# Performance work log

Hardware: AMD Instinct MI355X
Metric: run time of the kernel (lower is better)

Reference implementation:

```python
import jax, jax.numpy as jnp
import numpy as np
from jax import lax

H, W, C = 24, 8, 128
HW = H * W
PART = 4
SA_K = 49  # CBAM spatial-attention kernel size (default of CBAMBlock)
EPS = 1e-5


def conv2d(x, w, b, pad_h, pad_w):
    y = lax.conv_general_dilated(x, w, (1, 1), [(pad_h, pad_h), (pad_w, pad_w)],
                                 dimension_numbers=('NCHW', 'OIHW', 'NCHW'))
    return y + b[None, :, None, None]


def cbam(x, se_w1, se_w2, sa_w, sa_b):
    # Channel attention: shared MLP on global max- and avg-pooled descriptors.
    mx = x.max(axis=(2, 3))          # [n, c]
    av = x.mean(axis=(2, 3))         # [n, c]
    def se(v):
        return jax.nn.relu(v @ se_w1.T) @ se_w2.T
    ca = jax.nn.sigmoid(se(mx) + se(av))[:, :, None, None]
    out = x * ca
    # Spatial attention: 49x49 conv on [max, mean] over channels.
    smx = out.max(axis=1, keepdims=True)
    sav = out.mean(axis=1, keepdims=True)
    s = jnp.concatenate([smx, sav], axis=1)      # [n, 2, H, W]
    sa = jax.nn.sigmoid(conv2d(s, sa_w, sa_b, SA_K // 2, SA_K // 2))
    return out * sa + x


def position_aware_max(score6, dim):
    # score6: [p, g, hr, wr, hs, ws]; fixed-length (part_rows) row window,
    # start clamped to [0, h - part_rows] -> vectorized sliding-window max.
    part_rows = H // PART
    half = part_rows // 2
    starts = jnp.clip(jnp.arange(H) - half, 0, H - part_rows)
    if dim == 0:
        m = score6.max(axis=3)            # max over wr -> [p, g, hr, hs, ws]
        mi = jnp.moveaxis(m, 3, 0)        # [hs, p, g, hr, ws]
        def f(m_i, st):
            return lax.dynamic_slice_in_dim(m_i, st, part_rows, axis=2).max(axis=2)
        out = jax.vmap(f)(mi, starts)     # [h, p, g, ws]
    else:
        m = score6.max(axis=5)            # max over ws -> [p, g, hr, wr, hs]
        mi = jnp.moveaxis(m, 2, 0)        # [hr, p, g, wr, hs]
        def f(m_i, st):
            return lax.dynamic_slice_in_dim(m_i, st, part_rows, axis=3).max(axis=3)
        out = jax.vmap(f)(mi, starts)     # [h, p, g, wr]
    p, g = score6.shape[0], score6.shape[1]
    return jnp.moveaxis(out, 0, 2).reshape(p, g, HW)


def bn_eval(x, gamma, beta, mean, var):
    return (x - mean) * (gamma / jnp.sqrt(var + EPS)) + beta


def setup_inputs() -> dict:
    key = jax.random.key(0)
    ks = jax.random.split(key, 8)
    red = 16
    return {
        'prob_fea': jax.random.normal(ks[0], (32, C, H, W), jnp.float32),
        'gal_fea': jax.random.normal(ks[1], (32, C, H, W), jnp.float32),
        'se_w1': jax.random.normal(ks[2], (C // red, C), jnp.float32) * 0.05,
        'se_w2': jax.random.normal(ks[3], (C, C // red), jnp.float32) * 0.05,
        'sa_w': jax.random.normal(ks[4], (1, 2, SA_K, SA_K), jnp.float32) * 0.02,
        'sa_b': jnp.zeros((1,), jnp.float32),
        'bn_g': jnp.ones((1,), jnp.float32),
        'bn_b': jnp.zeros((1,), jnp.float32),
        'bn_m': jnp.zeros((1,), jnp.float32),
        'bn_v': jnp.ones((1,), jnp.float32),
        'fc_w': jnp.full((1, HW), 1.0 / HW, jnp.float32),
        'fc_b': jax.random.normal(ks[5], (1,), jnp.float32) * 0.01,
        'lbn_g': jnp.ones((1,), jnp.float32),
        'lbn_b': jnp.zeros((1,), jnp.float32),
        'lbn_m': jnp.zeros((1,), jnp.float32),
        'lbn_v': jnp.ones((1,), jnp.float32),
    }


def reference(prob_fea, gal_fea, se_w1, se_w2, sa_w, sa_b,
              bn_g, bn_b, bn_m, bn_v, fc_w, fc_b,
              lbn_g, lbn_b, lbn_m, lbn_v):
    pf = cbam(prob_fea, se_w1, se_w2, sa_w, sa_b)
    gf = cbam(gal_fea, se_w1, se_w2, sa_w, sa_b)
    p, g = pf.shape[0], gf.shape[0]
    pf = pf.reshape(p, C, HW)
    gf = gf.reshape(g, C, HW)
    # pairwise feature matching: [p, g, r(gal spatial), s(prob spatial)]
    score = jnp.einsum('pcs,gcr->pgrs', pf, gf)
    score6 = score.reshape(p, g, H, W, H, W)
    s1 = position_aware_max(score6, 0)  # [p, g, HW]
    s2 = position_aware_max(score6, 1)  # [p, g, HW]
    sc = jnp.concatenate([s1, s2], axis=-1).reshape(-1, HW)  # [p*g*2, HW]
    sc = bn_eval(sc, bn_g, bn_b, bn_m, bn_v)
    y = sc @ fc_w.T + fc_b                  # [p*g*2, 1]
    y = y.reshape(-1, 2).sum(axis=1, keepdims=True)
    y = bn_eval(y, lbn_g, lbn_b, lbn_m, lbn_v)
    return jax.nn.sigmoid(y).reshape(p, g)
```

## Files before the change

### kernel.cpp

```cpp
#include <hip/hip_runtime.h>
#include <hip/hip_bf16.h>

#define HH 24
#define WW 8
#define HWSZ 192
#define CC 128
#define EPSV 1e-5f

#define M1LD 200
#define M2LD 28

typedef __attribute__((ext_vector_type(8))) short bf16x8;
typedef __attribute__((ext_vector_type(4))) float f32x4;

__device__ __forceinline__ float sigmoidf_(float x) { return 1.0f / (1.0f + expf(-x)); }

__device__ __forceinline__ unsigned short f2bf(float f) {
    unsigned int u = __float_as_uint(f);
    unsigned int r = (u + 0x7fffu + ((u >> 16) & 1u)) >> 16;
    return (unsigned short)r;
}
__device__ __forceinline__ float bf2f(unsigned short s) {
    return __uint_as_float((unsigned int)s << 16);
}

__global__ __launch_bounds__(512) void cbam_stats(
    const float* __restrict__ prob, const float* __restrict__ gal,
    const float* __restrict__ se_w1, const float* __restrict__ se_w2,
    const float* __restrict__ sa_w, const float* __restrict__ sa_b,
    float* __restrict__ ca_out, float* __restrict__ sa_out)
{
    __shared__ float mxs[CC], avs[CC], hid[16], cas[CC];
    __shared__ float smx2[2 * HWSZ], sav2[2 * HWSZ];
    __shared__ float wbuf[2 * 49 * 49];

    int n = blockIdx.x;
    const float* x = (n < 32) ? prob + (size_t)n * CC * HWSZ : gal + (size_t)(n - 32) * CC * HWSZ;

    int tid = threadIdx.x, l = tid & 63, w = tid >> 6;

    for (int i = tid; i < 2 * 49 * 49; i += 512) wbuf[i] = sa_w[i];

    for (int i = 0; i < 16; ++i) {
        int c = w * 16 + i;
        const float* row = x + c * HWSZ;
        float a = row[l], b = row[l + 64], d = row[l + 128];
        float mv = fmaxf(a, fmaxf(b, d));
        float sv = a + b + d;
        #pragma unroll
        for (int m = 1; m < 64; m <<= 1) {
            mv = fmaxf(mv, __shfl_xor(mv, m));
            sv += __shfl_xor(sv, m);
        }
        if (l == 0) { mxs[c] = mv; avs[c] = sv * (1.0f / HWSZ); }
    }
    __syncthreads();

    if (tid < 256) {
        int j = tid >> 4, chunk = tid & 15;
        const float* v = (j < 8) ? mxs : avs;
        const float* wrow = se_w1 + (j & 7) * CC + chunk * 8;
        const float* vv = v + chunk * 8;
        float acc = 0.f;
        #pragma unroll
        for (int k = 0; k < 8; ++k) acc += vv[k] * wrow[k];
        #pragma unroll
        for (int m = 1; m < 16; m <<= 1) acc += __shfl_xor(acc, m);
        if (chunk == 0) hid[j] = fmaxf(acc, 0.f);
    }
    __syncthreads();

    if (tid < CC) {
        float acc = 0.f;
        #pragma unroll
        for (int j = 0; j < 8; ++j) acc += (hid[j] + hid[8 + j]) * se_w2[tid * 8 + j];
        cas[tid] = sigmoidf_(acc);
        ca_out[n * CC + tid] = cas[tid];
    }
    __syncthreads();

    if (tid < 2 * HWSZ) {
        int s = tid >> 1, half = tid & 1;
        int c0 = half * 64;
        float mv = -INFINITY, sv = 0.f;
        #pragma unroll 4
        for (int k = 0; k < 64; ++k) {
            float v = x[(c0 + k) * HWSZ + s] * cas[c0 + k];
            mv = fmaxf(mv, v); sv += v;
        }
        smx2[half * HWSZ + s] = mv; sav2[half * HWSZ + s] = sv;
    }
    __syncthreads();

    if (tid < HWSZ) {
        int y = tid >> 3, xx = tid & 7;
        float acc = sa_b[0];
        for (int iy = 0; iy < HH; ++iy) {
            int wy = iy - y + 24;
            const float* w0 = wbuf + wy * 49;
            const float* w1 = wbuf + 2401 + wy * 49;
            #pragma unroll
            for (int ix = 0; ix < WW; ++ix) {
                int wx = ix - xx + 24;
                int sp = iy * 8 + ix;
                float s0 = fmaxf(smx2[sp], smx2[HWSZ + sp]);
                float s1 = (sav2[sp] + sav2[HWSZ + sp]) * (1.0f / CC);
                acc += s0 * w0[wx] + s1 * w1[wx];
            }
        }
        sa_out[n * HWSZ + tid] = sigmoidf_(acc);
    }
}

__global__ __launch_bounds__(256) void cbam_apply(
    const float* __restrict__ prob, const float* __restrict__ gal,
    const float* __restrict__ ca_buf, const float* __restrict__ sa_buf,
    __hip_bfloat16* __restrict__ pf_t, __hip_bfloat16* __restrict__ gf_t)
{
    __shared__ unsigned short T[16][136];
    __shared__ float sash[16];

    int n = blockIdx.x / 12;
    int s0 = (blockIdx.x % 12) * 16;
    const float* x = (n < 32) ? prob + (size_t)n * CC * HWSZ : gal + (size_t)(n - 32) * CC * HWSZ;
    __hip_bfloat16* dst = (n < 32) ? pf_t + (size_t)n * HWSZ * CC : gf_t + (size_t)(n - 32) * HWSZ * CC;

    int tid = threadIdx.x;
    if (tid < 16) sash[tid] = sa_buf[n * HWSZ + s0 + tid];
    __syncthreads();

    int c = tid >> 1, half = tid & 1;
    float ca = ca_buf[n * CC + c];
    const float* xp = x + c * HWSZ + s0 + half * 8;
    float4 va = *(const float4*)xp;
    float4 vb = *(const float4*)(xp + 4);
    int r0 = half * 8;
    T[r0 + 0][c] = f2bf(va.x * (1.f + ca * sash[r0 + 0]));
    T[r0 + 1][c] = f2bf(va.y * (1.f + ca * sash[r0 + 1]));
    T[r0 + 2][c] = f2bf(va.z * (1.f + ca * sash[r0 + 2]));
    T[r0 + 3][c] = f2bf(va.w * (1.f + ca * sash[r0 + 3]));
    T[r0 + 4][c] = f2bf(vb.x * (1.f + ca * sash[r0 + 4]));
    T[r0 + 5][c] = f2bf(vb.y * (1.f + ca * sash[r0 + 5]));
    T[r0 + 6][c] = f2bf(vb.z * (1.f + ca * sash[r0 + 6]));
    T[r0 + 7][c] = f2bf(vb.w * (1.f + ca * sash[r0 + 7]));
    __syncthreads();

    int s_l = tid >> 4, c8 = (tid & 15) * 8;
    const unsigned int* src = (const unsigned int*)&T[s_l][c8];
    unsigned int* d32 = (unsigned int*)(dst + (s0 + s_l) * CC + c8);
    d32[0] = src[0]; d32[1] = src[1]; d32[2] = src[2]; d32[3] = src[3];
}

__global__ __launch_bounds__(384) void score_kernel(
    const __hip_bfloat16* __restrict__ pf_t, const __hip_bfloat16* __restrict__ gf_t,
    const float* __restrict__ bn_g, const float* __restrict__ bn_b,
    const float* __restrict__ bn_m, const float* __restrict__ bn_v,
    const float* __restrict__ fc_w, const float* __restrict__ fc_b,
    const float* __restrict__ lbn_g, const float* __restrict__ lbn_b,
    const float* __restrict__ lbn_m, const float* __restrict__ lbn_v,
    float* __restrict__ out)
{
    __shared__ __align__(16) char Bs[12 * 4096];
    __shared__ unsigned short M1b[24 * M1LD];
    __shared__ unsigned short M2b[HWSZ * M2LD];
    __shared__ float red[6], wred[6];

    int bi = blockIdx.x;
    int p = bi >> 5, g = bi & 31;
    int tid = threadIdx.x, l = tid & 63, w = tid >> 6;

    const __hip_bfloat16* A = gf_t + (size_t)g * HWSZ * CC;
    const __hip_bfloat16* B = pf_t + (size_t)p * HWSZ * CC;

    #pragma unroll
    for (int i = 0; i < 8; ++i) {
        int idx = w * 8 + i;
        const __hip_bfloat16* src = B + ((idx >> 2) * 16 + (l & 15)) * CC
                                      + ((idx & 3) * 4 + (l >> 4)) * 8;
        __builtin_amdgcn_global_load_lds(
            (const __attribute__((address_space(1))) void*)src,
            (__attribute__((address_space(3))) void*)(&Bs[idx * 1024]),
            16, 0, 0);
    }

    int row_a = l & 15;
    int koff = (l >> 4) * 8;
    bf16x8 afr[2][4];
    #pragma unroll
    for (int rt = 0; rt < 2; ++rt) {
        const __hip_bfloat16* ap = A + (w * 32 + rt * 16 + row_a) * CC + koff;
        #pragma unroll
        for (int ks = 0; ks < 4; ++ks)
            afr[rt][ks] = *(const bf16x8*)(ap + ks * 32);
    }
    __syncthreads();

    for (int st = 0; st < 12; ++st) {
        const char* bb = Bs + st * 4096;
        bf16x8 b0 = *(const bf16x8*)(bb + 0 * 1024 + l * 16);
        bf16x8 b1 = *(const bf16x8*)(bb + 1 * 1024 + l * 16);
        bf16x8 b2 = *(const bf16x8*)(bb + 2 * 1024 + l * 16);
        bf16x8 b3 = *(const bf16x8*)(bb + 3 * 1024 + l * 16);

        #pragma unroll
        for (int rt = 0; rt < 2; ++rt) {
            f32x4 acc1 = {0.f, 0.f, 0.f, 0.f};
            f32x4 acc2 = {0.f, 0.f, 0.f, 0.f};
            acc1 = __builtin_amdgcn_mfma_f32_16x16x32_bf16(afr[rt][0], b0, acc1, 0, 0, 0);
            acc2 = __builtin_amdgcn_mfma_f32_16x16x32_bf16(b0, afr[rt][0], acc2, 0, 0, 0);
            acc1 = __builtin_amdgcn_mfma_f32_16x16x32_bf16(afr[rt][1], b1, acc1, 0, 0, 0);
            acc2 = __builtin_amdgcn_mfma_f32_16x16x32_bf16(b1, afr[rt][1], acc2, 0, 0, 0);
            acc1 = __builtin_amdgcn_mfma_f32_16x16x32_bf16(afr[rt][2], b2, acc1, 0, 0, 0);
            acc2 = __builtin_amdgcn_mfma_f32_16x16x32_bf16(b2, afr[rt][2], acc2, 0, 0, 0);
            acc1 = __builtin_amdgcn_mfma_f32_16x16x32_bf16(afr[rt][3], b3, acc1, 0, 0, 0);
            acc2 = __builtin_amdgcn_mfma_f32_16x16x32_bf16(b3, afr[rt][3], acc2, 0, 0, 0);

            int RT = w * 2 + rt;

            float mrow = fmaxf(fmaxf(acc1[0], acc1[1]), fmaxf(acc1[2], acc1[3]));
            mrow = fmaxf(mrow, __shfl_xor(mrow, 16));
            if (((l >> 4) & 1) == 0)
                M1b[(2 * RT + (l >> 5)) * M1LD + st * 16 + (l & 15)] = f2bf(mrow);

            float mcol = fmaxf(fmaxf(acc2[0], acc2[1]), fmaxf(acc2[2], acc2[3]));
            mcol = fmaxf(mcol, __shfl_xor(mcol, 16));
            if (((l >> 4) & 1) == 0)
                M2b[(RT * 16 + (l & 15)) * M2LD + st * 2 + (l >> 5)] = f2bf(mcol);
        }
    }
    __syncthreads();

    float part = 0.f, wpart = 0.f;
    if (tid < HWSZ) {
        int h = tid >> 3;
        int st0 = h - 3; if (st0 < 0) st0 = 0; if (st0 > 18) st0 = 18;
        float v1 = -INFINITY, v2 = -INFINITY;
        #pragma unroll
        for (int i = 0; i < 6; ++i) {
            v1 = fmaxf(v1, bf2f(M1b[(st0 + i) * M1LD + tid]));
            v2 = fmaxf(v2, bf2f(M2b[tid * M2LD + st0 + i]));
        }
        float fw = fc_w[tid];
        part = fw * (v1 + v2);
        wpart = fw;
    }
    #pragma unroll
    for (int m = 1; m < 64; m <<= 1) {
        part  += __shfl_xor(part, m);
        wpart += __shfl_xor(wpart, m);
    }
    if (l == 0) { red[w] = part; wred[w] = wpart; }
    __syncthreads();

    if (tid == 0) {
        float total = red[0] + red[1] + red[2] + red[3] + red[4] + red[5];
        float Wsum  = wred[0] + wred[1] + wred[2] + wred[3] + wred[4] + wred[5];
        float k1 = bn_g[0] * rsqrtf(bn_v[0] + EPSV);
        float Y = k1 * total + 2.f * ((bn_b[0] - k1 * bn_m[0]) * Wsum + fc_b[0]);
        float kl = lbn_g[0] * rsqrtf(lbn_v[0] + EPSV);
        float Z = (Y - lbn_m[0]) * kl + lbn_b[0];
        out[bi] = 1.f / (1.f + expf(-Z));
    }
}

extern "C" void kernel_launch(void* const* d_in, const int* in_sizes, int n_in,
                              void* d_out, int out_size, void* d_ws, size_t ws_size,
                              hipStream_t stream)
{
    const float* prob  = (const float*)d_in[0];
    const float* gal   = (const float*)d_in[1];
    const float* se_w1 = (const float*)d_in[2];
    const float* se_w2 = (const float*)d_in[3];
    const float* sa_w  = (const float*)d_in[4];
    const float* sa_b  = (const float*)d_in[5];
    const float* bn_g  = (const float*)d_in[6];
    const float* bn_b  = (const float*)d_in[7];
    const float* bn_m  = (const float*)d_in[8];
    const float* bn_v  = (const float*)d_in[9];
    const float* fc_w  = (const float*)d_in[10];
    const float* fc_b  = (const float*)d_in[11];
    const float* lbn_g = (const float*)d_in[12];
    const float* lbn_b = (const float*)d_in[13];
    const float* lbn_m = (const float*)d_in[14];
    const float* lbn_v = (const float*)d_in[15];

    __hip_bfloat16* pf_t = (__hip_bfloat16*)d_ws;
    __hip_bfloat16* gf_t = pf_t + (size_t)32 * HWSZ * CC;
    float* ca_buf = (float*)(gf_t + (size_t)32 * HWSZ * CC);
    float* sa_buf = ca_buf + 64 * CC;
    float* out = (float*)d_out;

    cbam_stats<<<64, 512, 0, stream>>>(prob, gal, se_w1, se_w2, sa_w, sa_b, ca_buf, sa_buf);
    cbam_apply<<<768, 256, 0, stream>>>(prob, gal, ca_buf, sa_buf, pf_t, gf_t);
    score_kernel<<<1024, 384, 0, stream>>>(pf_t, gf_t, bn_g, bn_b, bn_m, bn_v,
                                           fc_w, fc_b, lbn_g, lbn_b, lbn_m, lbn_v, out);
}
```

Before: 151.8 us.

## Switch score GEMM to 32x32x16 MFMA with direct global B loads

The score kernel now uses 32x32x16 bf16 MFMA tiles instead of 16x16x32. Each wave covers 32 gallery rows against 32-position prob tiles over 6 steps. The LDS staging buffer for the prob features is removed, so B fragments are read straight from global memory (likely L2-resident) and the leading barrier goes away. It also adds an occupancy hint to launch_bounds. The intent is fewer MFMA issues, less LDS use and higher occupancy, at the cost of more global-load latency inside the inner loop and a larger accumulator register footprint.

```diff
diff --git a/kernel.cpp b/kernel.cpp
--- a/kernel.cpp
+++ b/kernel.cpp
@@ -11,7 +11,7 @@
 #define M2LD 28
 
 typedef __attribute__((ext_vector_type(8))) short bf16x8;
-typedef __attribute__((ext_vector_type(4))) float f32x4;
+typedef __attribute__((ext_vector_type(16))) float f32x16;
 
 __device__ __forceinline__ float sigmoidf_(float x) { return 1.0f / (1.0f + expf(-x)); }
 
@@ -151,7 +151,7 @@
     d32[0] = src[0]; d32[1] = src[1]; d32[2] = src[2]; d32[3] = src[3];
 }
 
-__global__ __launch_bounds__(384) void score_kernel(
+__global__ __launch_bounds__(384, 4) void score_kernel(
     const __hip_bfloat16* __restrict__ pf_t, const __hip_bfloat16* __restrict__ gf_t,
     const float* __restrict__ bn_g, const float* __restrict__ bn_b,
     const float* __restrict__ bn_m, const float* __restrict__ bn_v,
@@ -160,7 +160,6 @@
     const float* __restrict__ lbn_m, const float* __restrict__ lbn_v,
     float* __restrict__ out)
 {
-    __shared__ __align__(16) char Bs[12 * 4096];
     __shared__ unsigned short M1b[24 * M1LD];
     __shared__ unsigned short M2b[HWSZ * M2LD];
     __shared__ float red[6], wred[6];
@@ -172,60 +171,53 @@
     const __hip_bfloat16* A = gf_t + (size_t)g * HWSZ * CC;
     const __hip_bfloat16* B = pf_t + (size_t)p * HWSZ * CC;
 
-    #pragma unroll
-    for (int i = 0; i < 8; ++i) {
-        int idx = w * 8 + i;
-        const __hip_bfloat16* src = B + ((idx >> 2) * 16 + (l & 15)) * CC
-                                      + ((idx & 3) * 4 + (l >> 4)) * 8;
-        __builtin_amdgcn_global_load_lds(
-            (const __attribute__((address_space(1))) void*)src,
-            (__attribute__((address_space(3))) void*)(&Bs[idx * 1024]),
-            16, 0, 0);
-    }
-
-    int row_a = l & 15;
-    int koff = (l >> 4) * 8;
-    bf16x8 afr[2][4];
-    #pragma unroll
-    for (int rt = 0; rt < 2; ++rt) {
-        const __hip_bfloat16* ap = A + (w * 32 + rt * 16 + row_a) * CC + koff;
-        #pragma unroll
-        for (int ks = 0; ks < 4; ++ks)
-            afr[rt][ks] = *(const bf16x8*)(ap + ks * 32);
-    }
-    __syncthreads();
-
-    for (int st = 0; st < 12; ++st) {
-        const char* bb = Bs + st * 4096;
-        bf16x8 b0 = *(const bf16x8*)(bb + 0 * 1024 + l * 16);
-        bf16x8 b1 = *(const bf16x8*)(bb + 1 * 1024 + l * 16);
-        bf16x8 b2 = *(const bf16x8*)(bb + 2 * 1024 + l * 16);
-        bf16x8 b3 = *(const bf16x8*)(bb + 3 * 1024 + l * 16);
-
-        #pragma unroll
-        for (int rt = 0; rt < 2; ++rt) {
-            f32x4 acc1 = {0.f, 0.f, 0.f, 0.f};
-            f32x4 acc2 = {0.f, 0.f, 0.f, 0.f};
-            acc1 = __builtin_amdgcn_mfma_f32_16x16x32_bf16(afr[rt][0], b0, acc1, 0, 0, 0);
-            acc2 = __builtin_amdgcn_mfma_f32_16x16x32_bf16(b0, afr[rt][0], acc2, 0, 0, 0);
-            acc1 = __builtin_amdgcn_mfma_f32_16x16x32_bf16(afr[rt][1], b1, acc1, 0, 0, 0);
-            acc2 = __builtin_amdgcn_mfma_f32_16x16x32_bf16(b1, afr[rt][1], acc2, 0, 0, 0);
-            acc1 = __builtin_amdgcn_mfma_f32_16x16x32_bf16(afr[rt][2], b2, acc1, 0, 0, 0);
-            acc2 = __builtin_amdgcn_mfma_f32_16x16x32_bf16(b2, afr[rt][2], acc2, 0, 0, 0);
-            acc1 = __builtin_amdgcn_mfma_f32_16x16x32_bf16(afr[rt][3], b3, acc1, 0, 0, 0);
-            acc2 = __builtin_amdgcn_mfma_f32_16x16x32_bf16(b3, afr[rt][3], acc2, 0, 0, 0);
-
-            int RT = w * 2 + rt;
-
-            float mrow = fmaxf(fmaxf(acc1[0], acc1[1]), fmaxf(acc1[2], acc1[3]));
-            mrow = fmaxf(mrow, __shfl_xor(mrow, 16));
-            if (((l >> 4) & 1) == 0)
-                M1b[(2 * RT + (l >> 5)) * M1LD + st * 16 + (l & 15)] = f2bf(mrow);
-
-            float mcol = fmaxf(fmaxf(acc2[0], acc2[1]), fmaxf(acc2[2], acc2[3]));
-            mcol = fmaxf(mcol, __shfl_xor(mcol, 16));
-            if (((l >> 4) & 1) == 0)
-                M2b[(RT * 16 + (l & 15)) * M2LD + st * 2 + (l >> 5)] = f2bf(mcol);
+    int r32 = l & 31;
+    int koff = (l >> 5) * 8;
+
+    bf16x8 afr[8];
+    {
+        const __hip_bfloat16* ap = A + (w * 32 + r32) * CC + koff;
+        #pragma unroll
+        for (int ks = 0; ks < 8; ++ks) afr[ks] = *(const bf16x8*)(ap + ks * 16);
+    }
+
+    const __hip_bfloat16* bp0 = B + r32 * CC + koff;
+
+    for (int st = 0; st < 6; ++st) {
+        const __hip_bfloat16* bp = bp0 + st * 32 * CC;
+        f32x16 acc1 = {};
+        f32x16 acc2 = {};
+        #pragma unroll
+        for (int ks = 0; ks < 8; ++ks) {
+            bf16x8 bfr = *(const bf16x8*)(bp + ks * 16);
+            acc1 = __builtin_amdgcn_mfma_f32_32x32x16_bf16(afr[ks], bfr, acc1, 0, 0, 0);
+            acc2 = __builtin_amdgcn_mfma_f32_32x32x16_bf16(bfr, afr[ks], acc2, 0, 0, 0);
+        }
+
+        #pragma unroll
+        for (int q = 0; q < 4; ++q) {
+            float m = fmaxf(fmaxf(acc1[4 * q + 0], acc1[4 * q + 1]),
+                            fmaxf(acc1[4 * q + 2], acc1[4 * q + 3]));
+            m = fmaxf(m, __shfl_xor(m, 32));
+            if (l < 32)
+                M1b[(w * 4 + q) * M1LD + st * 32 + l] = f2bf(m);
+        }
+
+        unsigned short pk0, pk1, pk2, pk3;
+        {
+            float m0 = fmaxf(fmaxf(acc2[0], acc2[1]), fmaxf(acc2[2], acc2[3]));
+            float m1 = fmaxf(fmaxf(acc2[4], acc2[5]), fmaxf(acc2[6], acc2[7]));
+            float m2 = fmaxf(fmaxf(acc2[8], acc2[9]), fmaxf(acc2[10], acc2[11]));
+            float m3 = fmaxf(fmaxf(acc2[12], acc2[13]), fmaxf(acc2[14], acc2[15]));
+            m0 = fmaxf(m0, __shfl_xor(m0, 32));
+            m1 = fmaxf(m1, __shfl_xor(m1, 32));
+            m2 = fmaxf(m2, __shfl_xor(m2, 32));
+            m3 = fmaxf(m3, __shfl_xor(m3, 32));
+            pk0 = f2bf(m0); pk1 = f2bf(m1); pk2 = f2bf(m2); pk3 = f2bf(m3);
+        }
+        if (l < 32) {
+            ushort4 v; v.x = pk0; v.y = pk1; v.z = pk2; v.w = pk3;
+            *(ushort4*)(&M2b[(w * 32 + l) * M2LD + st * 4]) = v;
         }
     }
     __syncthreads();
```

Measured after the change: 155.3 us. 2.3% more time.

## Double-buffer probe feature staging in LDS and raise occupancy hint

Applied to the files above, without the earlier changes.

Replaces the single 48KB LDS load of the whole probe feature tile with a two-buffer ring of 12KB groups. The next group is prefetched while MFMAs run on the current one. This shrinks LDS per block so more blocks fit per CU, and the launch bound now requests 4 waves-per-EU occupancy. The cost is a barrier per group and possible register pressure from the occupancy hint.

```diff
diff --git a/kernel.cpp b/kernel.cpp
--- a/kernel.cpp
+++ b/kernel.cpp
@@ -151,7 +151,7 @@
     d32[0] = src[0]; d32[1] = src[1]; d32[2] = src[2]; d32[3] = src[3];
 }
 
-__global__ __launch_bounds__(384) void score_kernel(
+__global__ __launch_bounds__(384, 4) void score_kernel(
     const __hip_bfloat16* __restrict__ pf_t, const __hip_bfloat16* __restrict__ gf_t,
     const float* __restrict__ bn_g, const float* __restrict__ bn_b,
     const float* __restrict__ bn_m, const float* __restrict__ bn_v,
@@ -160,7 +160,7 @@
     const float* __restrict__ lbn_m, const float* __restrict__ lbn_v,
     float* __restrict__ out)
 {
-    __shared__ __align__(16) char Bs[12 * 4096];
+    __shared__ __align__(16) char bstage[2][3 * 4096];
     __shared__ unsigned short M1b[24 * M1LD];
     __shared__ unsigned short M2b[HWSZ * M2LD];
     __shared__ float red[6], wred[6];
@@ -172,16 +172,22 @@
     const __hip_bfloat16* A = gf_t + (size_t)g * HWSZ * CC;
     const __hip_bfloat16* B = pf_t + (size_t)p * HWSZ * CC;
 
-    #pragma unroll
-    for (int i = 0; i < 8; ++i) {
-        int idx = w * 8 + i;
-        const __hip_bfloat16* src = B + ((idx >> 2) * 16 + (l & 15)) * CC
-                                      + ((idx & 3) * 4 + (l >> 4)) * 8;
-        __builtin_amdgcn_global_load_lds(
-            (const __attribute__((address_space(1))) void*)src,
-            (__attribute__((address_space(3))) void*)(&Bs[idx * 1024]),
-            16, 0, 0);
-    }
+    #define STAGE_G(buf_, grp_)                                                          \
+        {                                                                                \
+            _Pragma("unroll")                                                            \
+            for (int i_ = 0; i_ < 2; ++i_) {                                             \
+                int idx_ = w * 2 + i_;                 \
+                const __hip_bfloat16* src_ = B + (((grp_) * 3 + (idx_ >> 2)) * 16        \
+                                                  + (l & 15)) * CC                       \
+                                               + ((idx_ & 3) * 4 + (l >> 4)) * 8;        \
+                __builtin_amdgcn_global_load_lds(                                        \
+                    (const __attribute__((address_space(1))) void*)src_,                 \
+                    (__attribute__((address_space(3))) void*)(&bstage[buf_][idx_ * 1024]),\
+                    16, 0, 0);                                                           \
+            }                                                                            \
+        }
+
+    STAGE_G(0, 0)
 
     int row_a = l & 15;
     int koff = (l >> 4) * 8;
@@ -195,40 +201,47 @@
     }
     __syncthreads();
 
-    for (int st = 0; st < 12; ++st) {
-        const char* bb = Bs + st * 4096;
-        bf16x8 b0 = *(const bf16x8*)(bb + 0 * 1024 + l * 16);
-        bf16x8 b1 = *(const bf16x8*)(bb + 1 * 1024 + l * 16);
-        bf16x8 b2 = *(const bf16x8*)(bb + 2 * 1024 + l * 16);
-        bf16x8 b3 = *(const bf16x8*)(bb + 3 * 1024 + l * 16);
-
-        #pragma unroll
-        for (int rt = 0; rt < 2; ++rt) {
-            f32x4 acc1 = {0.f, 0.f, 0.f, 0.f};
-            f32x4 acc2 = {0.f, 0.f, 0.f, 0.f};
-            acc1 = __builtin_amdgcn_mfma_f32_16x16x32_bf16(afr[rt][0], b0, acc1, 0, 0, 0);
-            acc2 = __builtin_amdgcn_mfma_f32_16x16x32_bf16(b0, afr[rt][0], acc2, 0, 0, 0);
-            acc1 = __builtin_amdgcn_mfma_f32_16x16x32_bf16(afr[rt][1], b1, acc1, 0, 0, 0);
-            acc2 = __builtin_amdgcn_mfma_f32_16x16x32_bf16(b1, afr[rt][1], acc2, 0, 0, 0);
-            acc1 = __builtin_amdgcn_mfma_f32_16x16x32_bf16(afr[rt][2], b2, acc1, 0, 0, 0);
-            acc2 = __builtin_amdgcn_mfma_f32_16x16x32_bf16(b2, afr[rt][2], acc2, 0, 0, 0);
-            acc1 = __builtin_amdgcn_mfma_f32_16x16x32_bf16(afr[rt][3], b3, acc1, 0, 0, 0);
-            acc2 = __builtin_amdgcn_mfma_f32_16x16x32_bf16(b3, afr[rt][3], acc2, 0, 0, 0);
-
-            int RT = w * 2 + rt;
-
-            float mrow = fmaxf(fmaxf(acc1[0], acc1[1]), fmaxf(acc1[2], acc1[3]));
-            mrow = fmaxf(mrow, __shfl_xor(mrow, 16));
-            if (((l >> 4) & 1) == 0)
-                M1b[(2 * RT + (l >> 5)) * M1LD + st * 16 + (l & 15)] = f2bf(mrow);
-
-            float mcol = fmaxf(fmaxf(acc2[0], acc2[1]), fmaxf(acc2[2], acc2[3]));
-            mcol = fmaxf(mcol, __shfl_xor(mcol, 16));
-            if (((l >> 4) & 1) == 0)
-                M2b[(RT * 16 + (l & 15)) * M2LD + st * 2 + (l >> 5)] = f2bf(mcol);
-        }
-    }
-    __syncthreads();
+    for (int grp = 0; grp < 4; ++grp) {
+        int cur = grp & 1;
+        if (grp < 3) STAGE_G(cur ^ 1, grp + 1)
+
+        #pragma unroll
+        for (int t = 0; t < 3; ++t) {
+            int st = grp * 3 + t;
+            const char* bb = bstage[cur] + t * 4096;
+            bf16x8 b0 = *(const bf16x8*)(bb + 0 * 1024 + l * 16);
+            bf16x8 b1 = *(const bf16x8*)(bb + 1 * 1024 + l * 16);
+            bf16x8 b2 = *(const bf16x8*)(bb + 2 * 1024 + l * 16);
+            bf16x8 b3 = *(const bf16x8*)(bb + 3 * 1024 + l * 16);
+
+            #pragma unroll
+            for (int rt = 0; rt < 2; ++rt) {
+                f32x4 acc1 = {0.f, 0.f, 0.f, 0.f};
+                f32x4 acc2 = {0.f, 0.f, 0.f, 0.f};
+                acc1 = __builtin_amdgcn_mfma_f32_16x16x32_bf16(afr[rt][0], b0, acc1, 0, 0, 0);
+                acc2 = __builtin_amdgcn_mfma_f32_16x16x32_bf16(b0, afr[rt][0], acc2, 0, 0, 0);
+                acc1 = __builtin_amdgcn_mfma_f32_16x16x32_bf16(afr[rt][1], b1, acc1, 0, 0, 0);
+                acc2 = __builtin_amdgcn_mfma_f32_16x16x32_bf16(b1, afr[rt][1], acc2, 0, 0, 0);
+                acc1 = __builtin_amdgcn_mfma_f32_16x16x32_bf16(afr[rt][2], b2, acc1, 0, 0, 0);
+                acc2 = __builtin_amdgcn_mfma_f32_16x16x32_bf16(b2, afr[rt][2], acc2, 0, 0, 0);
+                acc1 = __builtin_amdgcn_mfma_f32_16x16x32_bf16(afr[rt][3], b3, acc1, 0, 0, 0);
+                acc2 = __builtin_amdgcn_mfma_f32_16x16x32_bf16(b3, afr[rt][3], acc2, 0, 0, 0);
+
+                int RT = w * 2 + rt;
+
+                float mrow = fmaxf(fmaxf(acc1[0], acc1[1]), fmaxf(acc1[2], acc1[3]));
+                mrow = fmaxf(mrow, __shfl_xor(mrow, 16));
+                if (((l >> 4) & 1) == 0)
+                    M1b[(2 * RT + (l >> 5)) * M1LD + st * 16 + (l & 15)] = f2bf(mrow);
+
+                float mcol = fmaxf(fmaxf(acc2[0], acc2[1]), fmaxf(acc2[2], acc2[3]));
+                mcol = fmaxf(mcol, __shfl_xor(mcol, 16));
+                if (((l >> 4) & 1) == 0)
+                    M2b[(RT * 16 + (l & 15)) * M2LD + st * 2 + (l >> 5)] = f2bf(mcol);
+            }
+        }
+        __syncthreads();
+    }
 
     float part = 0.f, wpart = 0.f;
     if (tid < HWSZ) {
```

After: 137.9 us. 1.1x faster.
